# Optimization experiments

Hardware: AMD Instinct MI355X
Metric: run time of the kernel (lower is better)

## Reference

```python
import jax, jax.numpy as jnp
import numpy as np

B, T, E, H, V = 64, 64, 512, 512, 32000

def setup_inputs() -> dict:
    key = jax.random.key(0)
    ks = jax.random.split(key, 12)
    s_e = 1.0 / np.sqrt(E)
    s_h = 1.0 / np.sqrt(H)
    embed_table = jax.random.normal(ks[0], (V, E), jnp.float32) * 0.02
    embed_table = embed_table.at[0].set(0.0)  # padding_idx=0
    return {
        "enc_feats": jax.random.normal(ks[1], (B, E), jnp.float32),
        "captions": jax.random.randint(ks[2], (B, T), 1, V),
        "embed_table": embed_table,
        "W_ih": jax.random.normal(ks[3], (4 * H, E), jnp.float32) * s_e,
        "W_hh": jax.random.normal(ks[4], (4 * H, H), jnp.float32) * s_h,
        "b_ih": jax.random.normal(ks[5], (4 * H,), jnp.float32) * s_h,
        "b_hh": jax.random.normal(ks[6], (4 * H,), jnp.float32) * s_h,
        "Wh": jax.random.normal(ks[7], (H, E), jnp.float32) * s_e,
        "bh": jnp.zeros((H,), jnp.float32),
        "Wc": jax.random.normal(ks[8], (H, E), jnp.float32) * s_e,
        "bc": jnp.zeros((H,), jnp.float32),
        "Wout": jax.random.normal(ks[9], (V, H), jnp.float32) * s_h,
        "bout": jnp.zeros((V,), jnp.float32),
    }


def reference(enc_feats, captions, embed_table, W_ih, W_hh, b_ih, b_hh, Wh, bh, Wc, bc, Wout, bout):
    # Teacher-forced decode (forward_train, eval mode -> dropout is identity).
    inputs = captions[:, :-1]                       # [B, T-1]
    emb = embed_table[inputs]                       # [B, T-1, E]
    # Precompute input contribution to gates for all timesteps.
    xp = jnp.einsum("bte,ge->btg", emb, W_ih) + b_ih  # [B, T-1, 4H]
    xp = jnp.transpose(xp, (1, 0, 2))                 # [T-1, B, 4H]
    h0 = jnp.tanh(enc_feats @ Wh.T + bh)              # [B, H]
    c0 = jnp.tanh(enc_feats @ Wc.T + bc)              # [B, H]

    def step(carry, x_t):
        h, c = carry
        gates = x_t + h @ W_hh.T + b_hh               # [B, 4H]
        i, f, g, o = jnp.split(gates, 4, axis=-1)     # PyTorch gate order i,f,g,o
        i = jax.nn.sigmoid(i)
        f = jax.nn.sigmoid(f)
        g = jnp.tanh(g)
        o = jax.nn.sigmoid(o)
        c = f * c + i * g
        h = o * jnp.tanh(c)
        return (h, c), h

    _, hs = jax.lax.scan(step, (h0, c0), xp)          # hs: [T-1, B, H]
    logits = jnp.einsum("tbh,vh->btv", hs, Wout) + bout  # [B, T-1, V]
    return logits
```

## Files before the change

### kernel.cpp

```cpp
#include <hip/hip_runtime.h>
#include <hip/hip_bf16.h>
#include <stdint.h>
#include <math.h>

typedef __attribute__((ext_vector_type(4))) float f32x4;
typedef __attribute__((ext_vector_type(8))) short short8;

#define NB 64
#define NT 63
#define NE 512
#define NH 512
#define NV 32000
#define NG 2048
#define NBLK 16

__device__ __forceinline__ float sigm(float x) { return 1.f / (1.f + expf(-x)); }
__device__ __forceinline__ unsigned short f2b(float f) {
  union { float f; uint32_t u; } x; x.f = f;
  uint32_t r = x.u + 0x7FFF + ((x.u >> 16) & 1);
  return (unsigned short)(r >> 16);
}
__device__ __forceinline__ float b2f(unsigned short s) {
  union { uint32_t u; float f; } x; x.u = ((uint32_t)s) << 16; return x.f;
}
__device__ __forceinline__ f32x4 mfma16(short8 a, short8 b, f32x4 c) {
  return __builtin_amdgcn_mfma_f32_16x16x32_bf16(a, b, c, 0, 0, 0);
}

__global__ __launch_bounds__(256) void k_prep(
    const float* __restrict__ Wout, unsigned short* __restrict__ wb,
    unsigned short* __restrict__ hsb) {
  const int n4 = NV * NH / 4;
  for (int i = blockIdx.x * 256 + threadIdx.x; i < n4; i += gridDim.x * 256) {
    f32x4 v = *(const f32x4*)(Wout + (size_t)i * 4);
    unsigned short o[4];
#pragma unroll
    for (int u = 0; u < 4; ++u) o[u] = f2b(v[u]);
    *(uint64_t*)(wb + (size_t)i * 4) = *(const uint64_t*)o;
  }
  for (int i = blockIdx.x * 256 + threadIdx.x; i < 64 * NH; i += gridDim.x * 256)
    hsb[(size_t)(NT * NB) * NH + i] = 0;
}

__global__ __launch_bounds__(256) void k_prep2(
    const float* __restrict__ Whh, unsigned short* __restrict__ wp) {
  const int n4 = NG * NH / 4;
  for (int i4 = blockIdx.x * 256 + threadIdx.x; i4 < n4; i4 += gridDim.x * 256) {
    int r = i4 >> 7;
    int k4 = (i4 & 127) * 4;
    int np = 4 * (r & 511) + (r >> 9);
    f32x4 v = *(const f32x4*)(Whh + (size_t)r * NH + k4);
    unsigned short o[4];
#pragma unroll
    for (int u = 0; u < 4; ++u) o[u] = f2b(v[u]);
    *(uint64_t*)(wp + (size_t)np * NH + k4) = *(const uint64_t*)o;
  }
}

__global__ __launch_bounds__(256) void k_init(
    const float* __restrict__ enc, const float* __restrict__ Wh, const float* __restrict__ bh,
    const float* __restrict__ Wc, const float* __restrict__ bc,
    float* __restrict__ c0f, unsigned short* __restrict__ hAhi, unsigned short* __restrict__ hAlo) {
  int b = blockIdx.x;
  __shared__ float se[NE];
  for (int e = threadIdx.x; e < NE; e += 256) se[e] = enc[b * NE + e];
  __syncthreads();
  for (int j = threadIdx.x; j < NH; j += 256) {
    float dh = 0.f, dc = 0.f;
    const float* wh = Wh + (size_t)j * NE;
    const float* wc = Wc + (size_t)j * NE;
    for (int e = 0; e < NE; e += 4) {
      f32x4 vh = *(const f32x4*)(wh + e);
      f32x4 vc = *(const f32x4*)(wc + e);
#pragma unroll
      for (int u = 0; u < 4; ++u) {
        float x = se[e + u];
        dh += x * vh[u];
        dc += x * vc[u];
      }
    }
    float h = tanhf(dh + bh[j]);
    unsigned short hi = f2b(h);
    hAhi[b * NH + j] = hi;
    hAlo[b * NH + j] = f2b(h - b2f(hi));
    c0f[b * NH + j] = tanhf(dc + bc[j]);
  }
}

__global__ __launch_bounds__(256) void k_xp(
    const int* __restrict__ cap, const float* __restrict__ emb,
    const float* __restrict__ Wih, const float* __restrict__ bih, const float* __restrict__ bhh,
    float* __restrict__ xp) {
  int t = blockIdx.x;
  int g0 = blockIdx.y * 64;
  int b = threadIdx.x & 63;
  int gg = threadIdx.x >> 6;
  __shared__ float wl[64 * 32];

  int tok = cap[b * 64 + t];
  const float* er = emb + (size_t)tok * NE;

  float acc[16];
#pragma unroll
  for (int i = 0; i < 16; ++i) acc[i] = 0.f;

  for (int k0 = 0; k0 < NE; k0 += 32) {
    __syncthreads();
#pragma unroll
    for (int i = 0; i < 2; ++i) {
      int s = threadIdx.x + 256 * i;
      int gr = s >> 3, c4 = s & 7;
      *(f32x4*)(wl + gr * 32 + c4 * 4) =
          *(const f32x4*)(Wih + (size_t)(g0 + gr) * NE + k0 + c4 * 4);
    }
    __syncthreads();
    f32x4 e4[8];
#pragma unroll
    for (int u = 0; u < 8; ++u) e4[u] = *(const f32x4*)(er + k0 + u * 4);
#pragma unroll
    for (int k4 = 0; k4 < 8; ++k4) {
#pragma unroll
      for (int i = 0; i < 16; ++i) {
        f32x4 w = *(const f32x4*)(wl + (gg * 16 + i) * 32 + k4 * 4);
#pragma unroll
        for (int u = 0; u < 4; ++u) acc[i] += e4[k4][u] * w[u];
      }
    }
  }
  size_t rb = ((size_t)(t * NB) + b) * NG;
#pragma unroll
  for (int i = 0; i < 16; ++i) {
    int g = g0 + gg * 16 + i;
    int np = 4 * (g & 511) + (g >> 9);
    xp[rb + np] = acc[i] + bih[g] + bhh[g];
  }
}

__global__ __launch_bounds__(512, 1) void k_steps_p(
    const float* __restrict__ xp, const unsigned short* __restrict__ wp,
    unsigned short* __restrict__ hAhi, unsigned short* __restrict__ hAlo,
    unsigned short* __restrict__ hBhi, unsigned short* __restrict__ hBlo,
    const float* __restrict__ c0f, unsigned short* __restrict__ hsb,
    int* __restrict__ syncc) {
  int tid = threadIdx.x;
  int lane = tid & 63;
  int w = tid >> 6;
  int l15 = lane & 15;
  int kq = lane >> 4;
  int mloc = l15, ju = kq;
  int B = blockIdx.x;
  int J = B * 32 + w * 4 + ju;

  __shared__ unsigned short hh[64 * 512];
  __shared__ unsigned short hl[64 * 512];
  __shared__ float gb[8][272];

  float creg[4];
#pragma unroll
  for (int mi = 0; mi < 4; ++mi)
    creg[mi] = c0f[(size_t)(mi * 16 + mloc) * NH + J];

  for (int t = 0; t < NT; ++t) {
    const unsigned short* rhi = (t & 1) ? hBhi : hAhi;
    const unsigned short* rlo = (t & 1) ? hBlo : hAlo;
    unsigned short* whi2 = (t & 1) ? hAhi : hBhi;
    unsigned short* wlo2 = (t & 1) ? hAlo : hBlo;

#pragma unroll
    for (int q = 0; q < 8; ++q) {
      int m = q * 8 + w;
      int ke = lane * 8;
      int d = m * 512 + (ke ^ (8 * (m & 7)));
      *(short8*)(hh + d) = *(const short8*)(rhi + (size_t)m * 512 + ke);
      *(short8*)(hl + d) = *(const short8*)(rlo + (size_t)m * 512 + ke);
    }
    __syncthreads();

    f32x4 acc[4];
#pragma unroll
    for (int mi = 0; mi < 4; ++mi) acc[mi] = (f32x4){0.f, 0.f, 0.f, 0.f};
    const unsigned short* wpw = wp + ((size_t)B * 128 + w * 16 + l15) * 512;
    for (int ks = 0; ks < 16; ++ks) {
      int k = ks * 32 + kq * 8;
      short8 bf = *(const short8*)(wpw + k);
#pragma unroll
      for (int mi = 0; mi < 4; ++mi) {
        int m = mi * 16 + l15;
        int aoff = m * 512 + (k ^ (8 * (m & 7)));
        acc[mi] = mfma16(*(const short8*)(hh + aoff), bf, acc[mi]);
        acc[mi] = mfma16(*(const short8*)(hl + aoff), bf, acc[mi]);
      }
    }

    const float* xpt = xp + (size_t)t * NB * NG;
    unsigned short* hst = hsb + (size_t)t * NB * NH;
#pragma unroll
    for (int mi = 0; mi < 4; ++mi) {
#pragma unroll
      for (int r = 0; r < 4; ++r)
        gb[w][(kq * 4 + r) * 17 + l15] = acc[mi][r];
      int m = mi * 16 + mloc;
      float g0 = gb[w][mloc * 17 + ju * 4 + 0];
      float g1 = gb[w][mloc * 17 + ju * 4 + 1];
      float g2 = gb[w][mloc * 17 + ju * 4 + 2];
      float g3 = gb[w][mloc * 17 + ju * 4 + 3];
      f32x4 x4 = *(const f32x4*)(xpt + (size_t)m * NG + 4 * J);
      float gi = g0 + x4[0];
      float gf = g1 + x4[1];
      float gG = g2 + x4[2];
      float go = g3 + x4[3];
      float cn = sigm(gf) * creg[mi] + sigm(gi) * tanhf(gG);
      creg[mi] = cn;
      float h = sigm(go) * tanhf(cn);
      unsigned short hi = f2b(h);
      whi2[(size_t)m * NH + J] = hi;
      wlo2[(size_t)m * NH + J] = f2b(h - b2f(hi));
      hst[(size_t)m * NH + J] = hi;
    }

    if (t < NT - 1) {
      __syncthreads();
      if (tid == 0) {
        __threadfence();
        __hip_atomic_fetch_add(syncc, 1, __ATOMIC_RELEASE, __HIP_MEMORY_SCOPE_AGENT);
        while (__hip_atomic_load(syncc, __ATOMIC_ACQUIRE, __HIP_MEMORY_SCOPE_AGENT)
               < NBLK * (t + 1)) {}
        __threadfence();
      }
      __syncthreads();
    }
  }
}

__global__ __launch_bounds__(256) void k_logits_m(
    const unsigned short* __restrict__ hsb, const unsigned short* __restrict__ wb,
    const float* __restrict__ bout, float* __restrict__ out) {
  __shared__ unsigned short As[128 * 64];
  __shared__ unsigned short Bs[128 * 64];
  __shared__ float cst[4][16][68];
  int m0 = blockIdx.x * 128;
  int n0 = blockIdx.y * 128;
  int tid = threadIdx.x;
  int lane = tid & 63;
  int l15 = lane & 15;
  int kl = (lane >> 4) * 8;
  int w = tid >> 6;
  int wr = w >> 1, wc = w & 1;

  f32x4 acc[4][4];
#pragma unroll
  for (int i = 0; i < 4; ++i)
#pragma unroll
    for (int j = 0; j < 4; ++j) acc[i][j] = (f32x4){0.f, 0.f, 0.f, 0.f};

  for (int k0 = 0; k0 < NH; k0 += 64) {
    short8 ta[4], tb[4];
#pragma unroll
    for (int cc = 0; cc < 4; ++cc) {
      int idx = cc * 2048 + tid * 8;
      int row = idx >> 6;
      int ke = idx & 63;
      ta[cc] = *(const short8*)(hsb + (size_t)(m0 + row) * NH + k0 + ke);
      tb[cc] = *(const short8*)(wb + (size_t)(n0 + row) * NH + k0 + ke);
    }
    __syncthreads();
#pragma unroll
    for (int cc = 0; cc < 4; ++cc) {
      int idx = cc * 2048 + tid * 8;
      int row = idx >> 6;
      int ke = (idx & 63) ^ ((row & 7) << 3);
      *(short8*)(As + row * 64 + ke) = ta[cc];
      *(short8*)(Bs + row * 64 + ke) = tb[cc];
    }
    __syncthreads();
#pragma unroll
    for (int kk = 0; kk < 64; kk += 32) {
      short8 a[4], b[4];
#pragma unroll
      for (int mi = 0; mi < 4; ++mi) {
        int row = wr * 64 + mi * 16 + l15;
        a[mi] = *(const short8*)(As + row * 64 + ((kk + kl) ^ ((row & 7) << 3)));
      }
#pragma unroll
      for (int ni = 0; ni < 4; ++ni) {
        int row = wc * 64 + ni * 16 + l15;
        b[ni] = *(const short8*)(Bs + row * 64 + ((kk + kl) ^ ((row & 7) << 3)));
      }
#pragma unroll
      for (int mi = 0; mi < 4; ++mi)
#pragma unroll
        for (int ni = 0; ni < 4; ++ni)
          acc[mi][ni] = mfma16(a[mi], b[ni], acc[mi][ni]);
    }
  }

  f32x4 bo4 = *(const f32x4*)(bout + n0 + wc * 64 + l15 * 4);
#pragma unroll
  for (int mi = 0; mi < 4; ++mi) {
    __syncthreads();
#pragma unroll
    for (int ni = 0; ni < 4; ++ni)
#pragma unroll
      for (int r = 0; r < 4; ++r)
        cst[w][(lane >> 4) * 4 + r][ni * 16 + l15] = acc[mi][ni][r];
    __syncthreads();
#pragma unroll
    for (int p = 0; p < 4; ++p) {
      int row16 = p * 4 + (lane >> 4);
      int m = m0 + wr * 64 + mi * 16 + row16;
      f32x4 v = *(const f32x4*)&cst[w][row16][l15 * 4];
#pragma unroll
      for (int u = 0; u < 4; ++u) v[u] += bo4[u];
      if (m < NT * NB) {
        int t = m >> 6, b = m & 63;
        *(f32x4*)(out + (size_t)b * (NT * NV) + (size_t)t * NV + n0 + wc * 64 + l15 * 4) = v;
      }
    }
  }
}

extern "C" void kernel_launch(void* const* d_in, const int* in_sizes, int n_in,
                              void* d_out, int out_size, void* d_ws, size_t ws_size,
                              hipStream_t stream) {
  const float* enc  = (const float*)d_in[0];
  const int*   cap  = (const int*)d_in[1];
  const float* emb  = (const float*)d_in[2];
  const float* Wih  = (const float*)d_in[3];
  const float* Whh  = (const float*)d_in[4];
  const float* bih  = (const float*)d_in[5];
  const float* bhh  = (const float*)d_in[6];
  const float* Wh   = (const float*)d_in[7];
  const float* bh   = (const float*)d_in[8];
  const float* Wc   = (const float*)d_in[9];
  const float* bc   = (const float*)d_in[10];
  const float* Wout = (const float*)d_in[11];
  const float* bout = (const float*)d_in[12];
  float* out = (float*)d_out;

  char* ws = (char*)d_ws;
  constexpr size_t HA_HI = 0;
  constexpr size_t HA_LO = HA_HI + 65536;
  constexpr size_t HB_HI = HA_LO + 65536;
  constexpr size_t HB_LO = HB_HI + 65536;
  constexpr size_t HSB_OFF = HB_LO + 65536;
  constexpr size_t WB_OFF  = HSB_OFF + (size_t)4096 * NH * 2;
  constexpr size_t WP_OFF  = WB_OFF + (size_t)NV * NH * 2;
  constexpr size_t XP_OFF  = WP_OFF + (size_t)NG * NH * 2;
  unsigned short* hAhi = (unsigned short*)(ws + HA_HI);
  unsigned short* hAlo = (unsigned short*)(ws + HA_LO);
  unsigned short* hBhi = (unsigned short*)(ws + HB_HI);
  unsigned short* hBlo = (unsigned short*)(ws + HB_LO);
  float* c0f = (float*)(ws + HB_HI);
  unsigned short* hsb = (unsigned short*)(ws + HSB_OFF);
  unsigned short* wb  = (unsigned short*)(ws + WB_OFF);
  unsigned short* wp  = (unsigned short*)(ws + WP_OFF);
  float* xp = (float*)(ws + XP_OFF);
  int* syncc = (int*)(ws + HSB_OFF + (size_t)(NT * NB) * NH * 2);

  k_prep<<<1024, 256, 0, stream>>>(Wout, wb, hsb);
  k_prep2<<<256, 256, 0, stream>>>(Whh, wp);
  k_init<<<NB, 256, 0, stream>>>(enc, Wh, bh, Wc, bc, c0f, hAhi, hAlo);

  dim3 g2(NT, NG / 64);
  k_xp<<<g2, 256, 0, stream>>>(cap, emb, Wih, bih, bhh, xp);

  k_steps_p<<<NBLK, 512, 0, stream>>>(xp, wp, hAhi, hAlo, hBhi, hBlo, c0f, hsb, syncc);

  dim3 g4(32, NV / 128);
  k_logits_m<<<g4, 256, 0, stream>>>(hsb, wb, bout, out);
}
```

Measured before the change: 1.345 ms.

## Split LSTM recurrence across batch groups with per-group barriers

The persistent recurrent kernel now runs 64 blocks instead of 16. The batch is split into 4 independent groups of 16 rows, and each group has its own 16-block grid barrier counter. Each block stages only its 16 rows of h into shared memory and issues a quarter of the MFMAs per step. The point is to cut per-step latency and barrier contention on the serial critical path. The cost is that every W_hh slice is read by 4 blocks, and the kernel depends on all 64 blocks being co-resident and on the sync counters being zeroed with enough spacing.

Result: faster. 1.129 ms (-16.1%).

```diff
diff --git a/kernel.cpp b/kernel.cpp
--- a/kernel.cpp
+++ b/kernel.cpp
@@ -12,7 +12,8 @@
 #define NH 512
 #define NV 32000
 #define NG 2048
-#define NBLK 16
+#define GQ 4
+#define GS 16
 
 __device__ __forceinline__ float sigm(float x) { return 1.f / (1.f + expf(-x)); }
 __device__ __forceinline__ unsigned short f2b(float f) {
@@ -147,18 +148,20 @@
   int w = tid >> 6;
   int l15 = lane & 15;
   int kq = lane >> 4;
-  int mloc = l15, ju = kq;
-  int B = blockIdx.x;
-  int J = B * 32 + w * 4 + ju;
-
-  __shared__ unsigned short hh[64 * 512];
-  __shared__ unsigned short hl[64 * 512];
-  __shared__ float gb[8][272];
-
-  float creg[4];
-#pragma unroll
-  for (int mi = 0; mi < 4; ++mi)
-    creg[mi] = c0f[(size_t)(mi * 16 + mloc) * NH + J];
+  int q = blockIdx.x >> 4;
+  int s = blockIdx.x & 15;
+  int m0 = q * 16;
+  int ju = tid & 31;
+  int mu = tid >> 5;
+  int J = s * 32 + ju;
+
+  __shared__ unsigned short hh[16 * 512];
+  __shared__ unsigned short hl[16 * 512];
+  __shared__ float gb[128][17];
+
+  float creg = c0f[(size_t)(m0 + mu) * NH + J];
+  int* cnt = syncc + q * 32;
+  const unsigned short* wpw = wp + ((size_t)s * 128 + w * 16 + l15) * 512;
 
   for (int t = 0; t < NT; ++t) {
     const unsigned short* rhi = (t & 1) ? hBhi : hAhi;
@@ -166,65 +169,57 @@
     unsigned short* whi2 = (t & 1) ? hAhi : hBhi;
     unsigned short* wlo2 = (t & 1) ? hAlo : hBlo;
 
-#pragma unroll
-    for (int q = 0; q < 8; ++q) {
-      int m = q * 8 + w;
-      int ke = lane * 8;
+    f32x4 x4 = *(const f32x4*)(xp + ((size_t)t * NB + m0 + mu) * NG + 4 * J);
+
+#pragma unroll
+    for (int rdd = 0; rdd < 2; ++rdd) {
+      int idx = tid + rdd * 512;
+      int m = idx >> 6;
+      int ke = (idx & 63) * 8;
       int d = m * 512 + (ke ^ (8 * (m & 7)));
-      *(short8*)(hh + d) = *(const short8*)(rhi + (size_t)m * 512 + ke);
-      *(short8*)(hl + d) = *(const short8*)(rlo + (size_t)m * 512 + ke);
-    }
-    __syncthreads();
-
-    f32x4 acc[4];
-#pragma unroll
-    for (int mi = 0; mi < 4; ++mi) acc[mi] = (f32x4){0.f, 0.f, 0.f, 0.f};
-    const unsigned short* wpw = wp + ((size_t)B * 128 + w * 16 + l15) * 512;
+      *(short8*)(hh + d) = *(const short8*)(rhi + (size_t)(m0 + m) * 512 + ke);
+      *(short8*)(hl + d) = *(const short8*)(rlo + (size_t)(m0 + m) * 512 + ke);
+    }
+    __syncthreads();
+
+    f32x4 acc = (f32x4){0.f, 0.f, 0.f, 0.f};
     for (int ks = 0; ks < 16; ++ks) {
       int k = ks * 32 + kq * 8;
       short8 bf = *(const short8*)(wpw + k);
-#pragma unroll
-      for (int mi = 0; mi < 4; ++mi) {
-        int m = mi * 16 + l15;
-        int aoff = m * 512 + (k ^ (8 * (m & 7)));
-        acc[mi] = mfma16(*(const short8*)(hh + aoff), bf, acc[mi]);
-        acc[mi] = mfma16(*(const short8*)(hl + aoff), bf, acc[mi]);
-      }
-    }
-
-    const float* xpt = xp + (size_t)t * NB * NG;
-    unsigned short* hst = hsb + (size_t)t * NB * NH;
-#pragma unroll
-    for (int mi = 0; mi < 4; ++mi) {
-#pragma unroll
-      for (int r = 0; r < 4; ++r)
-        gb[w][(kq * 4 + r) * 17 + l15] = acc[mi][r];
-      int m = mi * 16 + mloc;
-      float g0 = gb[w][mloc * 17 + ju * 4 + 0];
-      float g1 = gb[w][mloc * 17 + ju * 4 + 1];
-      float g2 = gb[w][mloc * 17 + ju * 4 + 2];
-      float g3 = gb[w][mloc * 17 + ju * 4 + 3];
-      f32x4 x4 = *(const f32x4*)(xpt + (size_t)m * NG + 4 * J);
-      float gi = g0 + x4[0];
-      float gf = g1 + x4[1];
-      float gG = g2 + x4[2];
-      float go = g3 + x4[3];
-      float cn = sigm(gf) * creg[mi] + sigm(gi) * tanhf(gG);
-      creg[mi] = cn;
-      float h = sigm(go) * tanhf(cn);
-      unsigned short hi = f2b(h);
-      whi2[(size_t)m * NH + J] = hi;
-      wlo2[(size_t)m * NH + J] = f2b(h - b2f(hi));
-      hst[(size_t)m * NH + J] = hi;
-    }
+      int aoff = l15 * 512 + (k ^ (8 * (l15 & 7)));
+      acc = mfma16(*(const short8*)(hh + aoff), bf, acc);
+      acc = mfma16(*(const short8*)(hl + aoff), bf, acc);
+    }
+
+#pragma unroll
+    for (int r = 0; r < 4; ++r)
+      gb[w * 16 + l15][kq * 4 + r] = acc[r];
+    __syncthreads();
+
+    float g0 = gb[4 * ju + 0][mu];
+    float g1 = gb[4 * ju + 1][mu];
+    float g2 = gb[4 * ju + 2][mu];
+    float g3 = gb[4 * ju + 3][mu];
+    float gi = g0 + x4[0];
+    float gf = g1 + x4[1];
+    float gG = g2 + x4[2];
+    float go = g3 + x4[3];
+    float cn = sigm(gf) * creg + sigm(gi) * tanhf(gG);
+    creg = cn;
+    float h = sigm(go) * tanhf(cn);
+    unsigned short hi = f2b(h);
+    size_t hoff = (size_t)(m0 + mu) * NH + J;
+    whi2[hoff] = hi;
+    wlo2[hoff] = f2b(h - b2f(hi));
+    hsb[(size_t)t * NB * NH + hoff] = hi;
 
     if (t < NT - 1) {
       __syncthreads();
       if (tid == 0) {
         __threadfence();
-        __hip_atomic_fetch_add(syncc, 1, __ATOMIC_RELEASE, __HIP_MEMORY_SCOPE_AGENT);
-        while (__hip_atomic_load(syncc, __ATOMIC_ACQUIRE, __HIP_MEMORY_SCOPE_AGENT)
-               < NBLK * (t + 1)) {}
+        __hip_atomic_fetch_add(cnt, 1, __ATOMIC_RELEASE, __HIP_MEMORY_SCOPE_AGENT);
+        while (__hip_atomic_load(cnt, __ATOMIC_ACQUIRE, __HIP_MEMORY_SCOPE_AGENT)
+               < GS * (t + 1)) {}
         __threadfence();
       }
       __syncthreads();
@@ -364,7 +359,7 @@
   dim3 g2(NT, NG / 64);
   k_xp<<<g2, 256, 0, stream>>>(cap, emb, Wih, bih, bhh, xp);
 
-  k_steps_p<<<NBLK, 512, 0, stream>>>(xp, wp, hAhi, hAlo, hBhi, hBlo, c0f, hsb, syncc);
+  k_steps_p<<<GQ * GS, 512, 0, stream>>>(xp, wp, hAhi, hAlo, hBhi, hBlo, c0f, hsb, syncc);
 
   dim3 g4(32, NV / 128);
   k_logits_m<<<g4, 256, 0, stream>>>(hsb, wb, bout, out);
```
